# Performance work log

Hardware: AMD Instinct MI355X
Metric: run time of the kernel (lower is better)

Reference implementation:

```python
import jax, jax.numpy as jnp
import numpy as np

N_NODES = 100000
N_EDGES = 1600000
NUM_FEATURES = 32
EDGE_DIM = 8
GAT_DIM = 16
HEADS = 4
HID = GAT_DIM * HEADS  # 64
OUT_DIM = 2
NUM_GRAPHS = 64
NEG_SLOPE = 0.2


def setup_inputs() -> dict:
    key = jax.random.key(0)
    ks = jax.random.split(key, 24)
    g = lambda k, shp, fan: jax.random.normal(k, shp, jnp.float32) * (1.0 / np.sqrt(fan))
    inp = {
        'x': jax.random.normal(ks[0], (N_NODES, NUM_FEATURES), jnp.float32),
        'edge_index': jax.random.randint(ks[1], (2, N_EDGES), 0, N_NODES, jnp.int64),
        'edge_attr': jax.random.normal(ks[2], (N_EDGES, EDGE_DIM), jnp.float32),
        'batch': jnp.sort(jax.random.randint(ks[3], (N_NODES,), 0, NUM_GRAPHS, jnp.int64)),
        # input GATConv params (PyG: lin bias-free, att_* of shape [H,C], bias [H*C])
        'W0': g(ks[4], (NUM_FEATURES, HID), NUM_FEATURES),
        'att_src0': g(ks[5], (HEADS, GAT_DIM), GAT_DIM),
        'att_dst0': g(ks[6], (HEADS, GAT_DIM), GAT_DIM),
        'We0': g(ks[7], (EDGE_DIM, HID), EDGE_DIM),
        'att_e0': g(ks[8], (HEADS, GAT_DIM), GAT_DIM),
        'b0': jnp.zeros((HID,), jnp.float32),
        # 2 hidden GATConv layers, stacked on a leading layer axis
        'Wh': g(ks[9], (2, HID, HID), HID),
        'att_src_h': g(ks[10], (2, HEADS, GAT_DIM), GAT_DIM),
        'att_dst_h': g(ks[11], (2, HEADS, GAT_DIM), GAT_DIM),
        'We_h': g(ks[12], (2, EDGE_DIM, HID), EDGE_DIM),
        'att_e_h': g(ks[13], (2, HEADS, GAT_DIM), GAT_DIM),
        'bh': jnp.zeros((2, HID), jnp.float32),
        # MLP head
        'fc1_w': g(ks[14], (HID, 2 * GAT_DIM), HID),
        'fc1_b': jnp.zeros((2 * GAT_DIM,), jnp.float32),
        'fc2_w': g(ks[15], (2 * GAT_DIM, OUT_DIM), 2 * GAT_DIM),
        'fc2_b': jnp.zeros((OUT_DIM,), jnp.float32),
    }
    return inp


def _gat_conv(x, src, dst, ea, W, a_s, a_d, We, a_e, b, n_nodes):
    # x: [N, Fin] -> out: [N, H*C]
    xp = (x @ W).reshape(n_nodes, HEADS, GAT_DIM)
    al_s = jnp.einsum('nhc,hc->nh', xp, a_s)            # per-node src logits
    al_d = jnp.einsum('nhc,hc->nh', xp, a_d)
    ep = (ea @ We).reshape(-1, HEADS, GAT_DIM)
    al_e = jnp.einsum('ehc,hc->eh', ep, a_e)
    alpha = jax.nn.leaky_relu(al_s[src] + al_d[dst] + al_e, NEG_SLOPE)  # [E,H]
    m = jax.ops.segment_max(alpha, dst, num_segments=n_nodes)
    m = jnp.where(jnp.isfinite(m), m, 0.0)              # nodes with no in-edges
    ex = jnp.exp(alpha - m[dst])
    den = jax.ops.segment_sum(ex, dst, num_segments=n_nodes)
    coef = ex / (den[dst] + 1e-16)                      # segment softmax over dst
    out = jax.ops.segment_sum(xp[src] * coef[..., None], dst, num_segments=n_nodes)
    return out.reshape(n_nodes, HID) + b


def _forward(x, edge_index, edge_attr, batch, W0, att_src0, att_dst0, We0, att_e0,
             b0, Wh, att_src_h, att_dst_h, We_h, att_e_h, bh, fc1_w, fc1_b, fc2_w, fc2_b):
    n = x.shape[0]
    src, dst = edge_index[0], edge_index[1]
    # PyG add_self_loops(fill_value='mean'): self-loop attr = mean of incoming edge attrs
    cnt = jax.ops.segment_sum(jnp.ones((src.shape[0],), x.dtype), dst, num_segments=n)
    mean_attr = jax.ops.segment_sum(edge_attr, dst, num_segments=n) / jnp.clip(cnt, 1.0)[:, None]
    loop = jnp.arange(n, dtype=src.dtype)
    src_sl = jnp.concatenate([src, loop])
    dst_sl = jnp.concatenate([dst, loop])
    ea_sl = jnp.concatenate([edge_attr, mean_attr], axis=0)

    h = _gat_conv(x, src_sl, dst_sl, ea_sl, W0, att_src0, att_dst0, We0, att_e0, b0, n)
    h = jax.nn.relu(h)
    for i in range(2):  # source has `x - F.relu(x)` (no-op): no ReLU between hidden layers
        h = _gat_conv(h, src_sl, dst_sl, ea_sl, Wh[i], att_src_h[i], att_dst_h[i],
                      We_h[i], att_e_h[i], bh[i], n)
    # global_mean_pool over graphs
    ones = jnp.ones((n,), h.dtype)
    gcnt = jax.ops.segment_sum(ones, batch, num_segments=NUM_GRAPHS)
    pooled = jax.ops.segment_sum(h, batch, num_segments=NUM_GRAPHS) / jnp.clip(gcnt, 1.0)[:, None]
    y = jax.nn.relu(pooled @ fc1_w + fc1_b)
    return y @ fc2_w + fc2_b


def reference(x, edge_index, edge_attr, batch, W0, att_src0, att_dst0, We0, att_e0,
              b0, Wh, att_src_h, att_dst_h, We_h, att_e_h, bh, fc1_w, fc1_b, fc2_w, fc2_b):
    return _forward(x, edge_index, edge_attr, batch, W0, att_src0, att_dst0, We0, att_e0,
                    b0, Wh, att_src_h, att_dst_h, We_h, att_e_h, bh, fc1_w, fc1_b, fc2_w, fc2_b)
```

## Files before the change

kernel.cpp:

```cpp
#include <hip/hip_runtime.h>
#include <hip/hip_bf16.h>
#include <hip/hip_fp16.h>

#define N_NODES 100000
#define N_EDGES 1600000
#define E_SL (N_EDGES + N_NODES)
#define HID 64
#define NUM_GRAPHS 64
#define NEG_SLOPE 0.2f
#define SCAN_CHUNK 1024
#define SCAN_NB ((N_NODES + SCAN_CHUNK - 1) / SCAN_CHUNK)
#define ROW_W 8
#define XP_NODES_PER_BLK 16
#define POOL_NODES_PER_BLK 256
#define BUILD_NB (N_EDGES / 128)
#define XP0_NB (N_NODES / 16)


__global__ void hist_kernel(const int* __restrict__ ei, int* __restrict__ cnt,
                            int* __restrict__ rank) {
    int e = blockIdx.x * blockDim.x + threadIdx.x;
    if (e >= N_EDGES) return;
    rank[e] = atomicAdd(&cnt[ei[N_EDGES + e]], 1);
}

__global__ void scan_local_kernel(const int* __restrict__ cnt, int* __restrict__ row_ptr,
                                  int* __restrict__ bsum) {
    __shared__ int s[256];
    int t = threadIdx.x;
    int base = blockIdx.x * SCAN_CHUNK + t * 4;
    int v[4]; int sum = 0;
    #pragma unroll
    for (int i = 0; i < 4; ++i) {
        int idx = base + i;
        v[i] = (idx < N_NODES) ? cnt[idx] + 1 : 0;
        sum += v[i];
    }
    s[t] = sum;
    __syncthreads();
    for (int off = 1; off < 256; off <<= 1) {
        int x = (t >= off) ? s[t - off] : 0;
        __syncthreads();
        s[t] += x;
        __syncthreads();
    }
    int run = s[t] - sum;
    #pragma unroll
    for (int i = 0; i < 4; ++i) {
        int idx = base + i;
        if (idx < N_NODES) row_ptr[idx] = run;
        run += v[i];
    }
    if (t == 255) bsum[blockIdx.x] = s[255];
}

__global__ void scan_bsum_kernel(int* __restrict__ bsum) {
    if (threadIdx.x != 0) return;
    int acc = 0;
    for (int i = 0; i < SCAN_NB; ++i) { int v = bsum[i]; bsum[i] = acc; acc += v; }
}

__global__ void scan_add_kernel(int* __restrict__ row_ptr, const int* __restrict__ bsum) {
    int i = blockIdx.x * blockDim.x + threadIdx.x;
    if (i > N_NODES) return;
    if (i == N_NODES) row_ptr[i] = E_SL;
    else row_ptr[i] += bsum[i >> 10];
}

__global__ void weff_all_kernel(const float* __restrict__ We0, const float* __restrict__ ae0,
                                const float* __restrict__ Weh, const float* __restrict__ aeh,
                                float* __restrict__ weff) {
    int t = threadIdx.x;
    if (t >= 96) return;
    int layer = t >> 5, r = t & 31;
    int dd = r >> 2, h = r & 3;
    const float* We = (layer == 0) ? We0 : Weh + (size_t)(layer - 1) * 8 * 64;
    const float* ae = (layer == 0) ? ae0 : aeh + (size_t)(layer - 1) * 64;
    float s = 0.f;
    #pragma unroll
    for (int c = 0; c < 16; ++c) s += We[dd * 64 + h * 16 + c] * ae[h * 16 + c];
    weff[layer * 32 + dd * 4 + h] = s;
}

__global__ __launch_bounds__(256) void build_xp0_kernel(
    const int* __restrict__ ei, const float* __restrict__ ea,
    const int* __restrict__ row_ptr, const int* __restrict__ rank,
    const float* __restrict__ weff, unsigned int* __restrict__ ale_csr,
    const float* __restrict__ x, const float* __restrict__ W0,
    const float* __restrict__ a_s, const float* __restrict__ a_d,
    __half* __restrict__ xp, float* __restrict__ als, float* __restrict__ ald) {
    int b = blockIdx.x;
    int g = b / 3, r3 = b - g * 3;
    if (r3 == 2) {
        int wave = threadIdx.x >> 6, lane = threadIdx.x & 63;
        float wcol[32];
        #pragma unroll
        for (int k = 0; k < 32; ++k) wcol[k] = W0[k * 64 + lane];
        float asl = a_s[lane], adl = a_d[lane];
        int n0 = g * XP_NODES_PER_BLK + wave * 4;
        #pragma unroll 2
        for (int ni = 0; ni < 4; ++ni) {
            int n = n0 + ni;
            const float* xr = x + (size_t)n * 32;
            float a0 = 0.f, a1 = 0.f, a2 = 0.f, a3 = 0.f;
            #pragma unroll
            for (int k = 0; k < 32; k += 4) {
                float4 xv = *(const float4*)(xr + k);
                a0 += xv.x * wcol[k];     a1 += xv.y * wcol[k + 1];
                a2 += xv.z * wcol[k + 2]; a3 += xv.w * wcol[k + 3];
            }
            float acc = (a0 + a1) + (a2 + a3);
            xp[(size_t)n * 64 + lane] = __float2half(acc);
            float ps = acc * asl, pd = acc * adl;
            #pragma unroll
            for (int mk = 8; mk >= 1; mk >>= 1) {
                ps += __shfl_xor(ps, mk, 16);
                pd += __shfl_xor(pd, mk, 16);
            }
            if ((lane & 15) == 0) {
                als[(size_t)n * 4 + (lane >> 4)] = ps;
                ald[(size_t)n * 4 + (lane >> 4)] = pd;
            }
        }
        return;
    }
    int build_b = g * 2 + r3;
    int e = build_b * 128 + (threadIdx.x >> 1);
    int q = threadIdx.x & 1;
    int d = ei[N_EDGES + e];
    float4 a = *((const float4*)(ea + (size_t)e * 8) + q);
    float o0 = __shfl_xor(a.x, 1), o1 = __shfl_xor(a.y, 1);
    float o2 = __shfl_xor(a.z, 1), o3 = __shfl_xor(a.w, 1);
    float av[8];
    av[0] = q ? o0 : a.x;  av[1] = q ? o1 : a.y;
    av[2] = q ? o2 : a.z;  av[3] = q ? o3 : a.w;
    av[4] = q ? a.x : o0;  av[5] = q ? a.y : o1;
    av[6] = q ? a.z : o2;  av[7] = q ? a.w : o3;
    unsigned int w[4];
    if (q == 0) {
        float al[8];
        #pragma unroll
        for (int l = 0; l < 2; ++l) {
            #pragma unroll
            for (int h = 0; h < 4; ++h) {
                float s = 0.f;
                #pragma unroll
                for (int j = 0; j < 8; ++j) s += av[j] * weff[l * 32 + j * 4 + h];
                al[l * 4 + h] = s;
            }
        }
        __half2 p0 = __floats2half2_rn(al[0], al[1]);
        __half2 p1 = __floats2half2_rn(al[2], al[3]);
        __half2 p2 = __floats2half2_rn(al[4], al[5]);
        __half2 p3 = __floats2half2_rn(al[6], al[7]);
        w[0] = *(unsigned int*)&p0; w[1] = *(unsigned int*)&p1;
        w[2] = *(unsigned int*)&p2; w[3] = *(unsigned int*)&p3;
    } else {
        float al[4];
        #pragma unroll
        for (int h = 0; h < 4; ++h) {
            float s = 0.f;
            #pragma unroll
            for (int j = 0; j < 8; ++j) s += av[j] * weff[64 + j * 4 + h];
            al[h] = s;
        }
        __half2 p0 = __floats2half2_rn(al[0], al[1]);
        __half2 p1 = __floats2half2_rn(al[2], al[3]);
        w[0] = *(unsigned int*)&p0; w[1] = *(unsigned int*)&p1;
        w[2] = (unsigned int)ei[e];
        w[3] = 0u;
    }
    int pos = row_ptr[d] + rank[e];
    *(uint4*)(ale_csr + (size_t)pos * ROW_W + q * 4) =
        make_uint4(w[0], w[1], w[2], w[3]);
}

__global__ void mean_ea_kernel(const int* __restrict__ row_ptr,
                               unsigned int* __restrict__ ale_csr) {
    int idx = blockIdx.x * blockDim.x + threadIdx.x;
    if (idx >= N_NODES * 2) return;
    int n = idx >> 1, part = idx & 1;
    int start = row_ptr[n], last = row_ptr[n + 1] - 1;
    float inv = 1.f / fmaxf((float)(last - start), 1.f);
    if (part == 0) {
        float s[8] = {0.f, 0.f, 0.f, 0.f, 0.f, 0.f, 0.f, 0.f};
        for (int pos = start; pos < last; ++pos) {
            uint4 v = *(const uint4*)(ale_csr + (size_t)pos * ROW_W);
            float2 f0 = __half22float2(*(const __half2*)&v.x);
            float2 f1 = __half22float2(*(const __half2*)&v.y);
            float2 f2 = __half22float2(*(const __half2*)&v.z);
            float2 f3 = __half22float2(*(const __half2*)&v.w);
            s[0] += f0.x; s[1] += f0.y; s[2] += f1.x; s[3] += f1.y;
            s[4] += f2.x; s[5] += f2.y; s[6] += f3.x; s[7] += f3.y;
        }
        __half2 p0 = __floats2half2_rn(s[0] * inv, s[1] * inv);
        __half2 p1 = __floats2half2_rn(s[2] * inv, s[3] * inv);
        __half2 p2 = __floats2half2_rn(s[4] * inv, s[5] * inv);
        __half2 p3 = __floats2half2_rn(s[6] * inv, s[7] * inv);
        *(uint4*)(ale_csr + (size_t)last * ROW_W) =
            make_uint4(*(unsigned int*)&p0, *(unsigned int*)&p1,
                       *(unsigned int*)&p2, *(unsigned int*)&p3);
    } else {
        float s[4] = {0.f, 0.f, 0.f, 0.f};
        for (int pos = start; pos < last; ++pos) {
            uint2 v = *(const uint2*)(ale_csr + (size_t)pos * ROW_W + 4);
            float2 f0 = __half22float2(*(const __half2*)&v.x);
            float2 f1 = __half22float2(*(const __half2*)&v.y);
            s[0] += f0.x; s[1] += f0.y; s[2] += f1.x; s[3] += f1.y;
        }
        __half2 p0 = __floats2half2_rn(s[0] * inv, s[1] * inv);
        __half2 p1 = __floats2half2_rn(s[2] * inv, s[3] * inv);
        uint4 w = make_uint4(*(unsigned int*)&p0, *(unsigned int*)&p1,
                             (unsigned int)n, 0u);
        *(uint4*)(ale_csr + (size_t)last * ROW_W + 4) = w;
    }
}

template <bool FUSE_XP>
__global__ __launch_bounds__(256) void gat_node_kernel(
    const int* __restrict__ row_ptr, const unsigned int* __restrict__ ale_csr,
    const float* __restrict__ als, const float* __restrict__ ald,
    const __half* __restrict__ xp, int layer,
    float* __restrict__ out, const float* __restrict__ bias, int relu_flag,
    const float* __restrict__ Wn, const float* __restrict__ asn,
    const float* __restrict__ adn, __half* __restrict__ xpn,
    float* __restrict__ alsn, float* __restrict__ aldn) {
    __shared__ float exl[4 * 256];
    __shared__ int   coll[4 * 64];
    __shared__ float hrow[4 * 64];
    int wave = threadIdx.x >> 6, lane = threadIdx.x & 63;
    int node = blockIdx.x * 4 + wave;
    if (node >= N_NODES) return;
    int start = row_ptr[node], end = row_ptr[node + 1];
    int deg = end - start;
    int wb = wave * 64, wb4 = wave * 256;
    int cq = lane & 15;
    int eg = lane >> 4;
    int hv = cq >> 2;

    float4 ad4 = *(const float4*)(ald + (size_t)node * 4);

    float4 acc4 = make_float4(0.f, 0.f, 0.f, 0.f);
    float csum = 0.f;

    for (int base = 0; base < deg; base += 64) {
        int cnt = min(64, deg - base);
        float ex0 = 0.f, ex1 = 0.f, ex2 = 0.f, ex3 = 0.f;
        int s = 0;
        if (lane < cnt) {
            const unsigned int* row = ale_csr + (size_t)(start + base + lane) * ROW_W;
            uint2 alew = *(const uint2*)(row + 2 * layer);
            s = (int)row[6];
            float2 e01 = __half22float2(*(const __half2*)&alew.x);
            float2 e23 = __half22float2(*(const __half2*)&alew.y);
            float4 as4 = *(const float4*)(als + (size_t)s * 4);
            float v0 = as4.x + ad4.x + e01.x;
            float v1 = as4.y + ad4.y + e01.y;
            float v2 = as4.z + ad4.z + e23.x;
            float v3 = as4.w + ad4.w + e23.y;
            ex0 = expf((v0 >= 0.f) ? v0 : NEG_SLOPE * v0);
            ex1 = expf((v1 >= 0.f) ? v1 : NEG_SLOPE * v1);
            ex2 = expf((v2 >= 0.f) ? v2 : NEG_SLOPE * v2);
            ex3 = expf((v3 >= 0.f) ? v3 : NEG_SLOPE * v3);
        }
        *(float4*)(exl + wb4 + lane * 4) = make_float4(ex0, ex1, ex2, ex3);
        coll[wb + lane] = s;
        const float* exw = exl + wb4 + hv;
        int cntUp = (cnt + 15) & ~15;
        for (int j = eg; j < cntUp; j += 16) {
            int s0 = coll[wb + j],     s1 = coll[wb + j + 4];
            int s2 = coll[wb + j + 8], s3 = coll[wb + j + 12];
            float c0 = exw[(j) * 4],      c1 = exw[(j + 4) * 4];
            float c2 = exw[(j + 8) * 4],  c3 = exw[(j + 12) * 4];
            uint2 x0 = *(const uint2*)(xp + (size_t)s0 * 64 + cq * 4);
            uint2 x1 = *(const uint2*)(xp + (size_t)s1 * 64 + cq * 4);
            uint2 x2 = *(const uint2*)(xp + (size_t)s2 * 64 + cq * 4);
            uint2 x3 = *(const uint2*)(xp + (size_t)s3 * 64 + cq * 4);
            float2 f00 = __half22float2(*(const __half2*)&x0.x);
            float2 f01 = __half22float2(*(const __half2*)&x0.y);
            float2 f10 = __half22float2(*(const __half2*)&x1.x);
            float2 f11 = __half22float2(*(const __half2*)&x1.y);
            float2 f20 = __half22float2(*(const __half2*)&x2.x);
            float2 f21 = __half22float2(*(const __half2*)&x2.y);
            float2 f30 = __half22float2(*(const __half2*)&x3.x);
            float2 f31 = __half22float2(*(const __half2*)&x3.y);
            acc4.x += c0 * f00.x + c1 * f10.x + c2 * f20.x + c3 * f30.x;
            acc4.y += c0 * f00.y + c1 * f10.y + c2 * f20.y + c3 * f30.y;
            acc4.z += c0 * f01.x + c1 * f11.x + c2 * f21.x + c3 * f31.x;
            acc4.w += c0 * f01.y + c1 * f11.y + c2 * f21.y + c3 * f31.y;
            csum   += c0 + c1 + c2 + c3;
        }
    }
    #pragma unroll
    for (int mk = 16; mk < 64; mk <<= 1) {
        acc4.x += __shfl_xor(acc4.x, mk);
        acc4.y += __shfl_xor(acc4.y, mk);
        acc4.z += __shfl_xor(acc4.z, mk);
        acc4.w += __shfl_xor(acc4.w, mk);
        csum   += __shfl_xor(csum, mk);
    }
    float inv = 1.f / (csum + 1e-16f);
    float4 b4 = *(const float4*)(bias + cq * 4);
    float4 v;
    v.x = acc4.x * inv + b4.x;
    v.y = acc4.y * inv + b4.y;
    v.z = acc4.z * inv + b4.z;
    v.w = acc4.w * inv + b4.w;
    if (relu_flag) {
        v.x = fmaxf(v.x, 0.f); v.y = fmaxf(v.y, 0.f);
        v.z = fmaxf(v.z, 0.f); v.w = fmaxf(v.w, 0.f);
    }
    if (!FUSE_XP) {
        if (eg == 0)
            *(float4*)(out + (size_t)node * 64 + cq * 4) = v;
    } else {
        if (eg == 0) *(float4*)(hrow + wb + cq * 4) = v;
        float acc = 0.f;
        #pragma unroll
        for (int k0 = 0; k0 < 64; k0 += 8) {
            float wv[8];
            #pragma unroll
            for (int j = 0; j < 8; ++j) wv[j] = Wn[(k0 + j) * 64 + lane];
            #pragma unroll
            for (int j = 0; j < 8; ++j) acc += hrow[wb + k0 + j] * wv[j];
        }
        xpn[(size_t)node * 64 + lane] = __float2half(acc);
        float ps = acc * asn[lane], pd = acc * adn[lane];
        #pragma unroll
        for (int mk = 8; mk >= 1; mk >>= 1) {
            ps += __shfl_xor(ps, mk, 16);
            pd += __shfl_xor(pd, mk, 16);
        }
        if ((lane & 15) == 0) {
            alsn[(size_t)node * 4 + (lane >> 4)] = ps;
            aldn[(size_t)node * 4 + (lane >> 4)] = pd;
        }
    }
}

__global__ void pool_kernel(const float* __restrict__ h, const int* __restrict__ batch,
                            float* __restrict__ pooled) {
    int base = blockIdx.x * POOL_NODES_PER_BLK;
    int tid = threadIdx.x;
    int c = tid & 63, r = tid >> 6;
    float acc = 0.f;
    int curg = -1;
    for (int i = r; i < POOL_NODES_PER_BLK; i += 4) {
        int n = base + i;
        if (n >= N_NODES) break;
        int g = batch[n];
        if (g != curg) {
            if (curg >= 0) atomicAdd(&pooled[curg * 64 + c], acc);
            curg = g; acc = 0.f;
        }
        acc += h[(size_t)n * 64 + c];
    }
    if (curg >= 0) atomicAdd(&pooled[curg * 64 + c], acc);
}

__global__ void mlp_kernel(const float* __restrict__ pooled, const int* __restrict__ batch,
                           const float* __restrict__ w1, const float* __restrict__ b1,
                           const float* __restrict__ w2, const float* __restrict__ b2,
                           float* __restrict__ y) {
    int g = blockIdx.x, t = threadIdx.x;
    __shared__ float p[64], f1[32];
    __shared__ float invc_s;
    if (t == 0) {
        int lo = 0, hi = N_NODES;
        while (lo < hi) { int mid = (lo + hi) >> 1; if (batch[mid] < g) lo = mid + 1; else hi = mid; }
        int start = lo;
        hi = N_NODES;
        while (lo < hi) { int mid = (lo + hi) >> 1; if (batch[mid] < g + 1) lo = mid + 1; else hi = mid; }
        invc_s = 1.f / fmaxf((float)(lo - start), 1.f);
    }
    __syncthreads();
    p[t] = pooled[g * 64 + t] * invc_s;
    __syncthreads();
    if (t < 32) {
        float a = b1[t];
        #pragma unroll
        for (int k = 0; k < 64; ++k) a += p[k] * w1[k * 32 + t];
        f1[t] = fmaxf(a, 0.f);
    }
    __syncthreads();
    if (t < 2) {
        float a = b2[t];
        #pragma unroll
        for (int k = 0; k < 32; ++k) a += f1[k] * w2[k * 2 + t];
        y[g * 2 + t] = a;
    }
}

extern "C" void kernel_launch(void* const* d_in, const int* in_sizes, int n_in,
                              void* d_out, int out_size, void* d_ws, size_t ws_size,
                              hipStream_t stream) {
    const float* x    = (const float*)d_in[0];
    const int*   ei   = (const int*)d_in[1];
    const float* ea   = (const float*)d_in[2];
    const int*   batch= (const int*)d_in[3];
    const float* W0   = (const float*)d_in[4];
    const float* as0  = (const float*)d_in[5];
    const float* ad0  = (const float*)d_in[6];
    const float* We0  = (const float*)d_in[7];
    const float* ae0  = (const float*)d_in[8];
    const float* b0   = (const float*)d_in[9];
    const float* Wh   = (const float*)d_in[10];
    const float* ash  = (const float*)d_in[11];
    const float* adh  = (const float*)d_in[12];
    const float* Weh  = (const float*)d_in[13];
    const float* aeh  = (const float*)d_in[14];
    const float* bh   = (const float*)d_in[15];
    const float* w1   = (const float*)d_in[16];
    const float* b1   = (const float*)d_in[17];
    const float* w2   = (const float*)d_in[18];
    const float* b2   = (const float*)d_in[19];
    float* out = (float*)d_out;

    char* wsb = (char*)d_ws;
    size_t off = 0;
    auto alloc = [&](size_t bytes) { char* p = wsb + off; off += (bytes + 255) & ~(size_t)255; return p; };
    int*          row_ptr = (int*)alloc((size_t)(N_NODES + 1) * 4);
    unsigned int* ale_csr = (unsigned int*)alloc((size_t)E_SL * ROW_W * 4);
    float*        als0_b  = (float*)alloc((size_t)N_NODES * 4 * 4);
    float*        ald0_b  = (float*)alloc((size_t)N_NODES * 4 * 4);
    float*        als1_b  = (float*)alloc((size_t)N_NODES * 4 * 4);
    float*        ald1_b  = (float*)alloc((size_t)N_NODES * 4 * 4);
    float*        weff    = (float*)alloc(3 * 32 * 4);
    float*        pooled  = (float*)alloc((size_t)NUM_GRAPHS * 64 * 4);
    __half*       xpb0    = (__half*)alloc((size_t)N_NODES * 64 * 2);
    __half*       xpb1    = (__half*)alloc((size_t)N_NODES * 64 * 2);
    float*        bufB    = (float*)alloc((size_t)N_NODES * 64 * 4);
    int* cnt  = (int*)bufB;
    int* bsum = cnt + N_NODES;
    int* rank = bsum + ((SCAN_NB + 63) & ~63);

    float* alsb[2] = {als0_b, als1_b};
    float* aldb[2] = {ald0_b, ald1_b};
    __half* xpb[2] = {xpb0, xpb1};

    weff_all_kernel<<<1, 128, 0, stream>>>(We0, ae0, Weh, aeh, weff);
    hipMemsetAsync(cnt, 0, (size_t)N_NODES * 4, stream);
    hist_kernel<<<(N_EDGES + 255) / 256, 256, 0, stream>>>(ei, cnt, rank);
    scan_local_kernel<<<SCAN_NB, 256, 0, stream>>>(cnt, row_ptr, bsum);
    scan_bsum_kernel<<<1, 64, 0, stream>>>(bsum);
    scan_add_kernel<<<(N_NODES + 256) / 256, 256, 0, stream>>>(row_ptr, bsum);
    build_xp0_kernel<<<BUILD_NB + XP0_NB, 256, 0, stream>>>(
        ei, ea, row_ptr, rank, weff, ale_csr,
        x, W0, as0, ad0, xpb[0], alsb[0], aldb[0]);
    mean_ea_kernel<<<(N_NODES * 2 + 255) / 256, 256, 0, stream>>>(row_ptr, ale_csr);

    int gat_grid = (N_NODES + 3) / 4;
    gat_node_kernel<true><<<gat_grid, 256, 0, stream>>>(
        row_ptr, ale_csr, alsb[0], aldb[0], xpb[0], 0,
        nullptr, b0, 1,
        Wh, ash, adh, xpb[1], alsb[1], aldb[1]);
    gat_node_kernel<true><<<gat_grid, 256, 0, stream>>>(
        row_ptr, ale_csr, alsb[1], aldb[1], xpb[1], 1,
        nullptr, bh, 0,
        Wh + (size_t)64 * 64, ash + 64, adh + 64, xpb[0], alsb[0], aldb[0]);
    gat_node_kernel<false><<<gat_grid, 256, 0, stream>>>(
        row_ptr, ale_csr, alsb[0], aldb[0], xpb[0], 2,
        bufB, bh + 64, 0,
        nullptr, nullptr, nullptr, nullptr, nullptr, nullptr);

    hipMemsetAsync(pooled, 0, (size_t)NUM_GRAPHS * 64 * 4, stream);
    pool_kernel<<<(N_NODES + POOL_NODES_PER_BLK - 1) / POOL_NODES_PER_BLK, 256, 0, stream>>>(
        bufB, batch, pooled);
    mlp_kernel<<<NUM_GRAPHS, 64, 0, stream>>>(pooled, batch, w1, b1, w2, b2, out);
}
```

Before: 615.0 us.

## Compute self-loop attention inline in GAT kernel, drop mean edge-attr pass

Removes the separate mean_ea kernel and the self-loop rows from the CSR. Each GAT node kernel now computes the self-loop edge logit as the mean of its incoming edge logits, which equals the mean edge attribute projected by the linear map, and adds the self term to the accumulator directly. It also switches expf to the faster __expf intrinsic. This cuts a kernel launch, a full CSR pass and the extra rows, at the cost of slightly lower exp precision and a few more shuffles per node.

```diff
diff --git a/kernel.cpp b/kernel.cpp
--- a/kernel.cpp
+++ b/kernel.cpp
@@ -4,7 +4,6 @@
 
 #define N_NODES 100000
 #define N_EDGES 1600000
-#define E_SL (N_EDGES + N_NODES)
 #define HID 64
 #define NUM_GRAPHS 64
 #define NEG_SLOPE 0.2f
@@ -33,7 +32,7 @@
     #pragma unroll
     for (int i = 0; i < 4; ++i) {
         int idx = base + i;
-        v[i] = (idx < N_NODES) ? cnt[idx] + 1 : 0;
+        v[i] = (idx < N_NODES) ? cnt[idx] : 0;
         sum += v[i];
     }
     s[t] = sum;
@@ -63,7 +62,7 @@
 __global__ void scan_add_kernel(int* __restrict__ row_ptr, const int* __restrict__ bsum) {
     int i = blockIdx.x * blockDim.x + threadIdx.x;
     if (i > N_NODES) return;
-    if (i == N_NODES) row_ptr[i] = E_SL;
+    if (i == N_NODES) row_ptr[i] = N_EDGES;
     else row_ptr[i] += bsum[i >> 10];
 }
 
@@ -173,47 +172,6 @@
     int pos = row_ptr[d] + rank[e];
     *(uint4*)(ale_csr + (size_t)pos * ROW_W + q * 4) =
         make_uint4(w[0], w[1], w[2], w[3]);
-}
-
-__global__ void mean_ea_kernel(const int* __restrict__ row_ptr,
-                               unsigned int* __restrict__ ale_csr) {
-    int idx = blockIdx.x * blockDim.x + threadIdx.x;
-    if (idx >= N_NODES * 2) return;
-    int n = idx >> 1, part = idx & 1;
-    int start = row_ptr[n], last = row_ptr[n + 1] - 1;
-    float inv = 1.f / fmaxf((float)(last - start), 1.f);
-    if (part == 0) {
-        float s[8] = {0.f, 0.f, 0.f, 0.f, 0.f, 0.f, 0.f, 0.f};
-        for (int pos = start; pos < last; ++pos) {
-            uint4 v = *(const uint4*)(ale_csr + (size_t)pos * ROW_W);
-            float2 f0 = __half22float2(*(const __half2*)&v.x);
-            float2 f1 = __half22float2(*(const __half2*)&v.y);
-            float2 f2 = __half22float2(*(const __half2*)&v.z);
-            float2 f3 = __half22float2(*(const __half2*)&v.w);
-            s[0] += f0.x; s[1] += f0.y; s[2] += f1.x; s[3] += f1.y;
-            s[4] += f2.x; s[5] += f2.y; s[6] += f3.x; s[7] += f3.y;
-        }
-        __half2 p0 = __floats2half2_rn(s[0] * inv, s[1] * inv);
-        __half2 p1 = __floats2half2_rn(s[2] * inv, s[3] * inv);
-        __half2 p2 = __floats2half2_rn(s[4] * inv, s[5] * inv);
-        __half2 p3 = __floats2half2_rn(s[6] * inv, s[7] * inv);
-        *(uint4*)(ale_csr + (size_t)last * ROW_W) =
-            make_uint4(*(unsigned int*)&p0, *(unsigned int*)&p1,
-                       *(unsigned int*)&p2, *(unsigned int*)&p3);
-    } else {
-        float s[4] = {0.f, 0.f, 0.f, 0.f};
-        for (int pos = start; pos < last; ++pos) {
-            uint2 v = *(const uint2*)(ale_csr + (size_t)pos * ROW_W + 4);
-            float2 f0 = __half22float2(*(const __half2*)&v.x);
-            float2 f1 = __half22float2(*(const __half2*)&v.y);
-            s[0] += f0.x; s[1] += f0.y; s[2] += f1.x; s[3] += f1.y;
-        }
-        __half2 p0 = __floats2half2_rn(s[0] * inv, s[1] * inv);
-        __half2 p1 = __floats2half2_rn(s[2] * inv, s[3] * inv);
-        uint4 w = make_uint4(*(unsigned int*)&p0, *(unsigned int*)&p1,
-                             (unsigned int)n, 0u);
-        *(uint4*)(ale_csr + (size_t)last * ROW_W + 4) = w;
-    }
 }
 
 template <bool FUSE_XP>
@@ -238,10 +196,12 @@
     int eg = lane >> 4;
     int hv = cq >> 2;
 
-    float4 ad4 = *(const float4*)(ald + (size_t)node * 4);
+    float4 ad4  = *(const float4*)(ald + (size_t)node * 4);
+    float4 asn4 = *(const float4*)(als + (size_t)node * 4);
 
     float4 acc4 = make_float4(0.f, 0.f, 0.f, 0.f);
     float csum = 0.f;
+    float sm0 = 0.f, sm1 = 0.f, sm2 = 0.f, sm3 = 0.f;
 
     for (int base = 0; base < deg; base += 64) {
         int cnt = min(64, deg - base);
@@ -253,15 +213,16 @@
             s = (int)row[6];
             float2 e01 = __half22float2(*(const __half2*)&alew.x);
             float2 e23 = __half22float2(*(const __half2*)&alew.y);
+            sm0 += e01.x; sm1 += e01.y; sm2 += e23.x; sm3 += e23.y;
             float4 as4 = *(const float4*)(als + (size_t)s * 4);
             float v0 = as4.x + ad4.x + e01.x;
             float v1 = as4.y + ad4.y + e01.y;
             float v2 = as4.z + ad4.z + e23.x;
             float v3 = as4.w + ad4.w + e23.y;
-            ex0 = expf((v0 >= 0.f) ? v0 : NEG_SLOPE * v0);
-            ex1 = expf((v1 >= 0.f) ? v1 : NEG_SLOPE * v1);
-            ex2 = expf((v2 >= 0.f) ? v2 : NEG_SLOPE * v2);
-            ex3 = expf((v3 >= 0.f) ? v3 : NEG_SLOPE * v3);
+            ex0 = __expf((v0 >= 0.f) ? v0 : NEG_SLOPE * v0);
+            ex1 = __expf((v1 >= 0.f) ? v1 : NEG_SLOPE * v1);
+            ex2 = __expf((v2 >= 0.f) ? v2 : NEG_SLOPE * v2);
+            ex3 = __expf((v3 >= 0.f) ? v3 : NEG_SLOPE * v3);
         }
         *(float4*)(exl + wb4 + lane * 4) = make_float4(ex0, ex1, ex2, ex3);
         coll[wb + lane] = s;
@@ -292,6 +253,34 @@
         }
     }
     #pragma unroll
+    for (int mk = 1; mk < 64; mk <<= 1) {
+        sm0 += __shfl_xor(sm0, mk);
+        sm1 += __shfl_xor(sm1, mk);
+        sm2 += __shfl_xor(sm2, mk);
+        sm3 += __shfl_xor(sm3, mk);
+    }
+    float minv = 1.f / (float)max(deg, 1);
+    float sv0 = asn4.x + ad4.x + sm0 * minv;
+    float sv1 = asn4.y + ad4.y + sm1 * minv;
+    float sv2 = asn4.z + ad4.z + sm2 * minv;
+    float sv3 = asn4.w + ad4.w + sm3 * minv;
+    float exs0 = __expf((sv0 >= 0.f) ? sv0 : NEG_SLOPE * sv0);
+    float exs1 = __expf((sv1 >= 0.f) ? sv1 : NEG_SLOPE * sv1);
+    float exs2 = __expf((sv2 >= 0.f) ? sv2 : NEG_SLOPE * sv2);
+    float exs3 = __expf((sv3 >= 0.f) ? sv3 : NEG_SLOPE * sv3);
+    float exsl = (hv < 2) ? ((hv == 0) ? exs0 : exs1)
+                          : ((hv == 2) ? exs2 : exs3);
+    if (eg == 0) {
+        uint2 xn = *(const uint2*)(xp + (size_t)node * 64 + cq * 4);
+        float2 g0 = __half22float2(*(const __half2*)&xn.x);
+        float2 g1 = __half22float2(*(const __half2*)&xn.y);
+        acc4.x += exsl * g0.x;
+        acc4.y += exsl * g0.y;
+        acc4.z += exsl * g1.x;
+        acc4.w += exsl * g1.y;
+        csum   += exsl;
+    }
+    #pragma unroll
     for (int mk = 16; mk < 64; mk <<= 1) {
         acc4.x += __shfl_xor(acc4.x, mk);
         acc4.y += __shfl_xor(acc4.y, mk);
@@ -420,7 +409,7 @@
     size_t off = 0;
     auto alloc = [&](size_t bytes) { char* p = wsb + off; off += (bytes + 255) & ~(size_t)255; return p; };
     int*          row_ptr = (int*)alloc((size_t)(N_NODES + 1) * 4);
-    unsigned int* ale_csr = (unsigned int*)alloc((size_t)E_SL * ROW_W * 4);
+    unsigned int* ale_csr = (unsigned int*)alloc((size_t)N_EDGES * ROW_W * 4);
     float*        als0_b  = (float*)alloc((size_t)N_NODES * 4 * 4);
     float*        ald0_b  = (float*)alloc((size_t)N_NODES * 4 * 4);
     float*        als1_b  = (float*)alloc((size_t)N_NODES * 4 * 4);
@@ -447,7 +436,6 @@
     build_xp0_kernel<<<BUILD_NB + XP0_NB, 256, 0, stream>>>(
         ei, ea, row_ptr, rank, weff, ale_csr,
         x, W0, as0, ad0, xpb[0], alsb[0], aldb[0]);
-    mean_ea_kernel<<<(N_NODES * 2 + 255) / 256, 256, 0, stream>>>(row_ptr, ale_csr);
 
     int gat_grid = (N_NODES + 3) / 4;
     gat_node_kernel<true><<<gat_grid, 256, 0, stream>>>(
```

Result: faster. 593.6 us (-3.5%).
